# Kernel optimization log

Hardware: AMD Instinct MI355X
Metric: run time of the kernel (lower is better)

Reference implementation:

```python
import jax, jax.numpy as jnp
import numpy as np

N = 50000          # nodes
E = 1250000        # edges (no self loops in raw data)
H = 2              # heads
C = 32             # out channels per head
DIN = 64           # dim_node
ED = 16            # edge_dim
G = 16             # graphs in batch
NC = 5             # num classes
SLOPE = 0.2        # GATConv leaky_relu negative_slope


def _glorot(key, shape):
    fan = shape[0] if len(shape) == 2 else shape[-1]
    return jax.random.normal(key, shape, jnp.float32) * (1.0 / np.sqrt(fan))


def setup_inputs() -> dict:
    key = jax.random.key(0)
    ks = jax.random.split(key, 24)
    x = jax.random.normal(ks[0], (N, DIN), jnp.float32)
    dst = jax.random.randint(ks[1], (E,), 0, N)
    off = jax.random.randint(ks[2], (E,), 1, N)
    src = (dst + off) % N  # guarantees src != dst (PyG removes self loops before re-adding)
    edge_index = jnp.stack([src, dst]).astype(jnp.int32)
    edge_attr = jax.random.normal(ks[3], (E, ED), jnp.float32)
    batch = jnp.sort(jax.random.randint(ks[4], (N,), 0, G)).astype(jnp.int32)
    inp = dict(x=x, edge_index=edge_index, edge_attr=edge_attr, batch=batch)
    # layer 1: in=DIN, heads=H, out=C, concat -> H*C
    inp["W1"] = _glorot(ks[5], (DIN, H * C)); inp["asrc1"] = _glorot(ks[6], (H, C))
    inp["adst1"] = _glorot(ks[7], (H, C)); inp["We1"] = _glorot(ks[8], (ED, H * C))
    inp["ae1"] = _glorot(ks[9], (H, C)); inp["b1"] = jnp.zeros((H * C,), jnp.float32)
    # layer 2: in=H*C, heads=H, out=C, concat
    inp["W2"] = _glorot(ks[10], (H * C, H * C)); inp["asrc2"] = _glorot(ks[11], (H, C))
    inp["adst2"] = _glorot(ks[12], (H, C)); inp["We2"] = _glorot(ks[13], (ED, H * C))
    inp["ae2"] = _glorot(ks[14], (H, C)); inp["b2"] = jnp.zeros((H * C,), jnp.float32)
    # layer 3: in=H*C, heads=1, out=C, concat=False
    inp["W3"] = _glorot(ks[15], (H * C, C)); inp["asrc3"] = _glorot(ks[16], (1, C))
    inp["adst3"] = _glorot(ks[17], (1, C)); inp["We3"] = _glorot(ks[18], (ED, C))
    inp["ae3"] = _glorot(ks[19], (1, C)); inp["b3"] = jnp.zeros((C,), jnp.float32)
    # ffn: Linear(C, NC) + softmax (dropout is identity in eval)
    inp["Wf"] = _glorot(ks[20], (C, NC)); inp["bf"] = jnp.zeros((NC,), jnp.float32)
    return inp


def _gat_layer(h_in, src, dst, eattr, W, asrc, adst, We, ae, b, heads, out, concat):
    n = h_in.shape[0]
    h = (h_in @ W).reshape(n, heads, out)                      # [N,H,C]
    s_src = jnp.einsum('nhc,hc->nh', h, asrc)                  # per-node src scores
    s_dst = jnp.einsum('nhc,hc->nh', h, adst)
    he = (eattr @ We).reshape(-1, heads, out)                  # [E,H,C]
    s_e = jnp.einsum('ehc,hc->eh', he, ae)
    logit = jax.nn.leaky_relu(s_src[src] + s_dst[dst] + s_e, SLOPE)  # [E,H]
    m = jax.ops.segment_max(logit, dst, num_segments=n)
    ex = jnp.exp(logit - m[dst])
    den = jax.ops.segment_sum(ex, dst, num_segments=n)
    alpha = ex / (den[dst] + 1e-16)                            # segment softmax per dst node
    agg = jax.ops.segment_sum(h[src] * alpha[..., None], dst, num_segments=n)  # [N,H,C]
    out_x = agg.reshape(n, heads * out) if concat else agg.mean(axis=1)
    return out_x + b


def _gat_forward(x, edge_index, edge_attr, batch,
                 W1, asrc1, adst1, We1, ae1, b1,
                 W2, asrc2, adst2, We2, ae2, b2,
                 W3, asrc3, adst3, We3, ae3, b3,
                 Wf, bf):
    src, dst = edge_index[0], edge_index[1]
    n = x.shape[0]
    # add_self_loops with fill_value='mean': self-loop edge_attr = mean of incoming edge_attr
    deg = jax.ops.segment_sum(jnp.ones((src.shape[0],), x.dtype), dst, num_segments=n)
    self_attr = jax.ops.segment_sum(edge_attr, dst, num_segments=n) / jnp.maximum(deg, 1.0)[:, None]
    loop = jnp.arange(n, dtype=src.dtype)
    src_a = jnp.concatenate([src, loop])
    dst_a = jnp.concatenate([dst, loop])
    eattr_a = jnp.concatenate([edge_attr, self_attr], axis=0)

    h = jax.nn.relu(_gat_layer(x, src_a, dst_a, eattr_a, W1, asrc1, adst1, We1, ae1, b1, H, C, True))
    h = jax.nn.relu(_gat_layer(h, src_a, dst_a, eattr_a, W2, asrc2, adst2, We2, ae2, b2, H, C, True))
    h = jax.nn.relu(_gat_layer(h, src_a, dst_a, eattr_a, W3, asrc3, adst3, We3, ae3, b3, 1, C, False))

    # global mean pool per graph
    cnt = jax.ops.segment_sum(jnp.ones((n,), h.dtype), batch, num_segments=G)
    pooled = jax.ops.segment_sum(h, batch, num_segments=G) / jnp.maximum(cnt, 1.0)[:, None]
    # ffn: Dropout (identity at eval) -> Linear -> Softmax(dim=1)
    return jax.nn.softmax(pooled @ Wf + bf, axis=1)


def reference(x, edge_index, edge_attr, batch,
              W1, asrc1, adst1, We1, ae1, b1,
              W2, asrc2, adst2, We2, ae2, b2,
              W3, asrc3, adst3, We3, ae3, b3,
              Wf, bf):
    return _gat_forward(x, edge_index, edge_attr, batch,
                        W1, asrc1, adst1, We1, ae1, b1,
                        W2, asrc2, adst2, We2, ae2, b2,
                        W3, asrc3, adst3, We3, ae3, b3,
                        Wf, bf)
```

## Files before the change

kernel.cpp:

```cpp
#include <hip/hip_runtime.h>
#include <math.h>

#define NN 50000
#define EE 1250000
#define GG 16
#define NCLS 5
#define NBIN 391
#define BINSHIFT 7
#define CAPB 3900

constexpr size_t AL(size_t x){ return (x + 255) & ~size_t(255); }
constexpr size_t OFF_ROWPTR = 0;
constexpr size_t OFF_CURS   = OFF_ROWPTR + AL((size_t)(NN+1)*4);
constexpr size_t OFF_SRCS   = OFF_CURS + AL(4096);
constexpr size_t OFF_SE12   = OFF_SRCS + AL((size_t)EE*2);
constexpr size_t OFF_SE34   = OFF_SE12 + AL((size_t)EE*4);
constexpr size_t OFF_SE5    = OFF_SE34 + AL((size_t)EE*4);
constexpr size_t OFF_SSRC   = OFF_SE5 + AL((size_t)EE*2);
constexpr size_t OFF_SDST   = OFF_SSRC + AL((size_t)NN*2*4);
constexpr size_t OFF_STAG   = OFF_SDST + AL((size_t)NN*2*4);
constexpr size_t OFF_BUFH   = OFF_STAG + AL((size_t)NBIN*CAPB*16);
constexpr size_t OFF_BUFO   = OFF_BUFH + AL((size_t)NN*32*4);
constexpr size_t OFF_WEFF   = OFF_BUFO + AL((size_t)NN*64*4);
constexpr size_t OFF_POOL   = OFF_WEFF + AL(80*4);

__device__ __forceinline__ float leaky(float x){ return x > 0.f ? x : 0.2f*x; }
__device__ __forceinline__ unsigned rne_bf16(float x){
    unsigned u = __float_as_uint(x);
    return (u + 0x7FFFu + ((u >> 16) & 1u)) >> 16;
}
__device__ __forceinline__ float bf16lo(unsigned p){ return __uint_as_float(p << 16); }
__device__ __forceinline__ float bf16hi(unsigned p){ return __uint_as_float(p & 0xFFFF0000u); }

__global__ void weffbinit_kernel(const float* __restrict__ We1, const float* __restrict__ ae1,
                                 const float* __restrict__ We2, const float* __restrict__ ae2,
                                 const float* __restrict__ We3, const float* __restrict__ ae3,
                                 float* __restrict__ weff, int* __restrict__ bincursor){
    int t = threadIdx.x;
    if (t < NBIN) bincursor[t] = t*CAPB;
    if (t >= 80) return;
    int j = t >> 4, d = t & 15;
    const float* We; const float* ae; int hc, h;
    if (j == 0){ We = We1; ae = ae1; hc = 64; h = 0; }
    else if (j == 1){ We = We1; ae = ae1; hc = 64; h = 1; }
    else if (j == 2){ We = We2; ae = ae2; hc = 64; h = 0; }
    else if (j == 3){ We = We2; ae = ae2; hc = 64; h = 1; }
    else { We = We3; ae = ae3; hc = 32; h = 0; }
    float s = 0.f;
    for (int c = 0; c < 32; ++c) s += We[d*hc + h*32 + c] * ae[h*32 + c];
    weff[j*16 + d] = s;
}

__global__ void binA_kernel(const int* __restrict__ src, const int* __restrict__ dst,
                            const float* __restrict__ eattr, const float* __restrict__ weff,
                            int* __restrict__ bincursor, int4* __restrict__ staging, int nE){
    __shared__ int lcount[NBIN];
    __shared__ int lbase[NBIN];
    __shared__ float w[80];
    int tid = threadIdx.x;
    if (tid < 80) w[tid] = weff[tid];
    for (int i = tid; i < NBIN; i += 1024) lcount[i] = 0;
    __syncthreads();
    int base = blockIdx.x * 2048;
    int w0[2], bn[2], idx[2]; unsigned p01[2], p23[2], p4[2];
    #pragma unroll
    for (int k = 0; k < 2; ++k){
        int i = base + k*1024 + tid;
        if (i < nE){
            int d = dst[i];
            int s = src[i];
            bn[k]  = d >> BINSHIFT;
            w0[k]  = s | ((d & 127) << 16);
            const float4* row = (const float4*)(eattr + (size_t)i*16);
            float4 a0 = row[0], a1 = row[1], a2 = row[2], a3 = row[3];
            float a[16] = {a0.x,a0.y,a0.z,a0.w, a1.x,a1.y,a1.z,a1.w,
                           a2.x,a2.y,a2.z,a2.w, a3.x,a3.y,a3.z,a3.w};
            float sj[5];
            #pragma unroll
            for (int j = 0; j < 5; ++j){
                float s2 = 0.f;
                #pragma unroll
                for (int d2 = 0; d2 < 16; ++d2) s2 += a[d2]*w[j*16+d2];
                sj[j] = s2;
            }
            p01[k] = rne_bf16(sj[0]) | (rne_bf16(sj[1]) << 16);
            p23[k] = rne_bf16(sj[2]) | (rne_bf16(sj[3]) << 16);
            p4[k]  = rne_bf16(sj[4]);
            idx[k] = atomicAdd(&lcount[bn[k]], 1);
        } else bn[k] = -1;
    }
    __syncthreads();
    for (int i = tid; i < NBIN; i += 1024)
        lbase[i] = atomicAdd(&bincursor[i], lcount[i]);
    __syncthreads();
    #pragma unroll
    for (int k = 0; k < 2; ++k)
        if (bn[k] >= 0)
            staging[lbase[bn[k]] + idx[k]] = make_int4(w0[k], (int)p01[k], (int)p23[k], (int)p4[k]);
}

__global__ void binscan_kernel(const int* __restrict__ bincursor, int* __restrict__ binbase){
    __shared__ int s[512];
    int tid = threadIdx.x;
    int v = (tid < NBIN) ? (bincursor[tid] - tid*CAPB) : 0;
    s[tid] = v;
    __syncthreads();
    for (int off = 1; off < 512; off <<= 1){
        int t = (tid >= off) ? s[tid-off] : 0;
        __syncthreads();
        s[tid] += t;
        __syncthreads();
    }
    if (tid < NBIN) binbase[tid] = s[tid] - v;
}

__global__ void binB_kernel(const int* __restrict__ bincursor, const int* __restrict__ binbase,
                            const int4* __restrict__ staging,
                            unsigned short* __restrict__ srcs, unsigned* __restrict__ se12,
                            unsigned* __restrict__ se34, unsigned short* __restrict__ se5,
                            int* __restrict__ rowptr, int nN){
    __shared__ int4 lout[CAPB];
    __shared__ int lcnt[128];
    __shared__ int lpre[128];
    int b = blockIdx.x;
    int sbase = b*CAPB;
    int cnt = bincursor[b] - sbase;
    int tid = threadIdx.x;
    if (tid < 128) lcnt[tid] = 0;
    __syncthreads();
    for (int k = tid; k < cnt; k += 1024)
        atomicAdd(&lcnt[staging[sbase + k].x >> 16], 1);
    __syncthreads();
    if (tid < 64){
        int a0 = lcnt[2*tid], a1 = lcnt[2*tid+1];
        int pair = a0 + a1, incl = pair;
        #pragma unroll
        for (int off = 1; off < 64; off <<= 1){
            int t = __shfl_up(incl, off);
            if (tid >= off) incl += t;
        }
        int base0 = incl - pair;
        lpre[2*tid] = base0;
        lpre[2*tid+1] = base0 + a0;
    }
    __syncthreads();
    int r0 = binbase[b];
    int lo = b << BINSHIFT;
    if (tid < 128 && lo + tid < nN) rowptr[lo + tid] = r0 + lpre[tid];
    if (b == NBIN-1 && tid == 0) rowptr[nN] = r0 + cnt;
    if (tid < 128) lcnt[tid] = 0;
    __syncthreads();
    for (int k = tid; k < cnt; k += 1024){
        int4 v = staging[sbase + k];
        int dl = v.x >> 16;
        int rank = atomicAdd(&lcnt[dl], 1);
        v.x &= 0xFFFF;
        lout[lpre[dl] + rank] = v;
    }
    __syncthreads();
    for (int k = tid; k < cnt; k += 1024){
        int4 v = lout[k];
        srcs[r0 + k] = (unsigned short)v.x;
        se12[r0 + k] = (unsigned)v.y;
        se34[r0 + k] = (unsigned)v.z;
        se5[r0 + k]  = (unsigned short)v.w;
    }
}

template<int OUTC>
__global__ void transform_kernel(const float* __restrict__ in, const float* __restrict__ W,
                                 const float* __restrict__ asrc, const float* __restrict__ adst,
                                 unsigned* __restrict__ hout2, float* __restrict__ ssrc,
                                 float* __restrict__ sdst, int nN){
    constexpr int R = 256/OUTC;
    __shared__ float Ws[64*OUTC];
    __shared__ float ins[R*64];
    int tid = threadIdx.x;
    for (int i = tid; i < 64*OUTC; i += 256) Ws[i] = W[i];
    int base = blockIdx.x * R;
    for (int i = tid; i < R*64; i += 256){
        int n = base + i/64;
        ins[i] = (n < nN) ? in[(size_t)n*64 + (i & 63)] : 0.f;
    }
    __syncthreads();
    int r = tid / OUTC, c = tid % OUTC;
    int n = base + r;
    float acc = 0.f;
    #pragma unroll
    for (int d = 0; d < 64; ++d) acc += ins[r*64 + d] * Ws[d*OUTC + c];
    float ps = acc * asrc[c];
    float pd = acc * adst[c];
    #pragma unroll
    for (int m = 1; m <= 16; m <<= 1){ ps += __shfl_xor(ps, m); pd += __shfl_xor(pd, m); }
    float accN = __shfl_xor(acc, 1);
    if (n < nN){
        int h = c >> 5;
        if ((c & 1) == 0){
            unsigned pk = rne_bf16(acc) | (rne_bf16(accN) << 16);
            hout2[((size_t)h*nN + n)*16 + ((c & 31) >> 1)] = pk;
        }
        if ((c & 31) == 0){
            ssrc[(size_t)h*nN + n] = ps;
            sdst[(size_t)h*nN + n] = pd;
        }
    }
}

template<int MODE>
__global__ void aggH_kernel(const int* __restrict__ rowptr, const unsigned short* __restrict__ srcs,
                            const unsigned* __restrict__ sePa, const unsigned short* __restrict__ sePb,
                            const float* __restrict__ ssrcH, const float* __restrict__ sdstH,
                            const uint2* __restrict__ hb2, const float* __restrict__ bias,
                            float4* __restrict__ outb, int ostride4, int nN){
    int wid = threadIdx.x >> 6;
    int lane = threadIdx.x & 63;
    int n = blockIdx.x*4 + wid;
    if (n >= nN) return;
    int row_start = rowptr[n], row_end = rowptr[n+1];
    int degn = row_end - row_start;
    float sdh = sdstH[n];
    int q0 = lane >> 3, lc = lane & 7;

    float acc0=0.f, acc1=0.f, acc2=0.f, acc3=0.f, den=0.f, ssp=0.f;
    for (int p0 = row_start; p0 < row_end; p0 += 64){
        int myp = p0 + lane;
        unsigned wpk = 0;
        if (myp < row_end){
            int srcreg = srcs[myp];
            float e;
            if (MODE == 0)      e = __uint_as_float(((unsigned)sePb[myp]) << 16);
            else if (MODE == 1) e = bf16lo(sePa[myp]);
            else                e = bf16hi(sePa[myp]);
            ssp += e;
            float wv = __expf(leaky(ssrcH[srcreg] + sdh + e));
            wpk = (unsigned)srcreg | (rne_bf16(wv) << 16);
        }
        int cnt2 = min(64, row_end - p0);
        for (int qq = q0; qq < cnt2; qq += 8){
            unsigned u = __shfl(wpk, qq);
            int sj = u & 0xFFFF;
            float wj = __uint_as_float(u & 0xFFFF0000u);
            den += wj;
            uint2 hv = hb2[(size_t)sj*8 + lc];
            acc0 += wj * bf16lo(hv.x);
            acc1 += wj * bf16hi(hv.x);
            acc2 += wj * bf16lo(hv.y);
            acc3 += wj * bf16hi(hv.y);
        }
    }
    #pragma unroll
    for (int m = 1; m < 64; m <<= 1) ssp += __shfl_xor(ssp, m);
    #pragma unroll
    for (int m = 8; m < 64; m <<= 1){
        acc0 += __shfl_xor(acc0, m); acc1 += __shfl_xor(acc1, m);
        acc2 += __shfl_xor(acc2, m); acc3 += __shfl_xor(acc3, m);
        den  += __shfl_xor(den, m);
    }
    float invdeg = 1.f / (float)max(degn, 1);
    float wself = __expf(leaky(ssrcH[n] + sdh + ssp*invdeg));
    uint2 hv = hb2[(size_t)n*8 + lc];
    acc0 += wself * bf16lo(hv.x); acc1 += wself * bf16hi(hv.x);
    acc2 += wself * bf16lo(hv.y); acc3 += wself * bf16hi(hv.y);
    den += wself;
    if (lane < 8){
        float inv = 1.f / (den + 1e-16f);
        float4 o;
        o.x = fmaxf(acc0*inv + bias[4*lc+0], 0.f);
        o.y = fmaxf(acc1*inv + bias[4*lc+1], 0.f);
        o.z = fmaxf(acc2*inv + bias[4*lc+2], 0.f);
        o.w = fmaxf(acc3*inv + bias[4*lc+3], 0.f);
        outb[(size_t)n*ostride4 + lc] = o;
    }
}

__global__ void pool_kernel(const float* __restrict__ h3, const int* __restrict__ batch,
                            float* __restrict__ pool, float* __restrict__ cnt, int nN){
    __shared__ float accs[GG*32];
    __shared__ float acccnt[GG];
    int tid = threadIdx.x;
    for (int i = tid; i < GG*32; i += 256) accs[i] = 0.f;
    if (tid < GG) acccnt[tid] = 0.f;
    __syncthreads();
    int r = tid >> 5, c = tid & 31;
    int base = blockIdx.x * 512;
    int end = min(base + 512, nN);
    for (int n = base + r; n < end; n += 8){
        int g = batch[n];
        atomicAdd(&accs[g*32 + c], h3[(size_t)n*32 + c]);
        if (c == 0) atomicAdd(&acccnt[g], 1.f);
    }
    __syncthreads();
    for (int i = tid; i < GG*32; i += 256) atomicAdd(&pool[i], accs[i]);
    if (tid < GG) atomicAdd(&cnt[tid], acccnt[tid]);
}

__global__ void final_kernel(const float* __restrict__ pool, const float* __restrict__ cnt,
                             const float* __restrict__ Wf, const float* __restrict__ bf,
                             float* __restrict__ out){
    int g = threadIdx.x;
    if (g >= GG) return;
    float ic = 1.f / fmaxf(cnt[g], 1.f);
    float lg[NCLS];
    #pragma unroll
    for (int k = 0; k < NCLS; ++k) lg[k] = bf[k];
    for (int c = 0; c < 32; ++c){
        float v = pool[g*32 + c] * ic;
        #pragma unroll
        for (int k = 0; k < NCLS; ++k) lg[k] += v * Wf[c*NCLS + k];
    }
    float mx = lg[0];
    #pragma unroll
    for (int k = 1; k < NCLS; ++k) mx = fmaxf(mx, lg[k]);
    float sum = 0.f, ex[NCLS];
    #pragma unroll
    for (int k = 0; k < NCLS; ++k){ ex[k] = expf(lg[k] - mx); sum += ex[k]; }
    #pragma unroll
    for (int k = 0; k < NCLS; ++k) out[g*NCLS + k] = ex[k]/sum;
}

extern "C" void kernel_launch(void* const* d_in, const int* in_sizes, int n_in,
                              void* d_out, int out_size, void* d_ws, size_t ws_size,
                              hipStream_t stream){
    const float* x     = (const float*)d_in[0];
    const int*   eidx  = (const int*)d_in[1];
    const float* eattr = (const float*)d_in[2];
    const int*   batch = (const int*)d_in[3];
    const float* W1 = (const float*)d_in[4];  const float* asrc1 = (const float*)d_in[5];
    const float* adst1 = (const float*)d_in[6]; const float* We1 = (const float*)d_in[7];
    const float* ae1 = (const float*)d_in[8];  const float* b1 = (const float*)d_in[9];
    const float* W2 = (const float*)d_in[10]; const float* asrc2 = (const float*)d_in[11];
    const float* adst2 = (const float*)d_in[12]; const float* We2 = (const float*)d_in[13];
    const float* ae2 = (const float*)d_in[14]; const float* b2 = (const float*)d_in[15];
    const float* W3 = (const float*)d_in[16]; const float* asrc3 = (const float*)d_in[17];
    const float* adst3 = (const float*)d_in[18]; const float* We3 = (const float*)d_in[19];
    const float* ae3 = (const float*)d_in[20]; const float* b3 = (const float*)d_in[21];
    const float* Wf = (const float*)d_in[22]; const float* bf = (const float*)d_in[23];
    float* out = (float*)d_out;

    char* ws = (char*)d_ws;
    int*   rowptr = (int*)(ws + OFF_ROWPTR);
    int*   curs   = (int*)(ws + OFF_CURS);
    unsigned short* srcs = (unsigned short*)(ws + OFF_SRCS);
    unsigned* se12 = (unsigned*)(ws + OFF_SE12);
    unsigned* se34 = (unsigned*)(ws + OFF_SE34);
    unsigned short* se5 = (unsigned short*)(ws + OFF_SE5);
    float* ssrc   = (float*)(ws + OFF_SSRC);
    float* sdst   = (float*)(ws + OFF_SDST);
    int4*  staging = (int4*)(ws + OFF_STAG);
    unsigned* bufH = (unsigned*)(ws + OFF_BUFH);
    float* bufO   = (float*)(ws + OFF_BUFO);
    float* weff   = (float*)(ws + OFF_WEFF);
    float* pool   = (float*)(ws + OFF_POOL);
    float* cnt    = pool + GG*32;

    int* bincursor = curs;
    int* binbase   = curs + 512;

    const int* srcA = eidx;
    const int* dstA = eidx + EE;

    hipMemsetAsync(pool, 0, (GG*32 + GG)*4, stream);

    weffbinit_kernel<<<1, 512, 0, stream>>>(We1, ae1, We2, ae2, We3, ae3, weff, bincursor);
    binA_kernel<<<(EE + 2047)/2048, 1024, 0, stream>>>(srcA, dstA, eattr, weff, bincursor, staging, EE);
    binscan_kernel<<<1, 512, 0, stream>>>(bincursor, binbase);
    binB_kernel<<<NBIN, 1024, 0, stream>>>(bincursor, binbase, staging, srcs, se12, se34, se5, rowptr, NN);

    int ngrid4 = (NN + 3)/4;
    int ngrid8 = (NN + 7)/8;
    const uint2* hb = (const uint2*)bufH;
    float4* o4 = (float4*)bufO;
    transform_kernel<64><<<ngrid4, 256, 0, stream>>>(x, W1, asrc1, adst1, bufH, ssrc, sdst, NN);
    aggH_kernel<1><<<ngrid4, 256, 0, stream>>>(rowptr, srcs, se12, nullptr, ssrc,      sdst,      hb,          b1,      o4,     16, NN);
    aggH_kernel<2><<<ngrid4, 256, 0, stream>>>(rowptr, srcs, se12, nullptr, ssrc + NN, sdst + NN, hb + NN*8,   b1 + 32, o4 + 8, 16, NN);
    transform_kernel<64><<<ngrid4, 256, 0, stream>>>(bufO, W2, asrc2, adst2, bufH, ssrc, sdst, NN);
    aggH_kernel<1><<<ngrid4, 256, 0, stream>>>(rowptr, srcs, se34, nullptr, ssrc,      sdst,      hb,          b2,      o4,     16, NN);
    aggH_kernel<2><<<ngrid4, 256, 0, stream>>>(rowptr, srcs, se34, nullptr, ssrc + NN, sdst + NN, hb + NN*8,   b2 + 32, o4 + 8, 16, NN);
    transform_kernel<32><<<ngrid8, 256, 0, stream>>>(bufO, W3, asrc3, adst3, bufH, ssrc, sdst, NN);
    aggH_kernel<0><<<ngrid4, 256, 0, stream>>>(rowptr, srcs, nullptr, se5, ssrc, sdst, hb, b3, o4, 8, NN);
    pool_kernel<<<(NN + 511)/512, 256, 0, stream>>>(bufO, batch, pool, cnt, NN);
    final_kernel<<<1, 64, 0, stream>>>(pool, cnt, Wf, bf, out);
}
```

Measured before the change: 299.2 us.

## Fuse two-head aggregation into one kernel with node-major interleaved layout

Node features and attention scores are now stored node-major with both heads interleaved, so one aggregation kernel handles both heads per node. This replaces two per-head launches per layer, sharing the CSR walk, source-index and edge-score loads, and the exp computation across heads. Each edge is processed by fewer lanes in parallel because the lanes now cover a wider feature row. The edge binning kernel also handles four edges per thread and skips global atomics for empty bins.

```diff
diff --git a/kernel.cpp b/kernel.cpp
--- a/kernel.cpp
+++ b/kernel.cpp
@@ -61,10 +61,10 @@
     if (tid < 80) w[tid] = weff[tid];
     for (int i = tid; i < NBIN; i += 1024) lcount[i] = 0;
     __syncthreads();
-    int base = blockIdx.x * 2048;
-    int w0[2], bn[2], idx[2]; unsigned p01[2], p23[2], p4[2];
-    #pragma unroll
-    for (int k = 0; k < 2; ++k){
+    int base = blockIdx.x * 4096;
+    int w0[4], bn[4], idx[4]; unsigned p01[4], p23[4], p4[4];
+    #pragma unroll
+    for (int k = 0; k < 4; ++k){
         int i = base + k*1024 + tid;
         if (i < nE){
             int d = dst[i];
@@ -90,11 +90,13 @@
         } else bn[k] = -1;
     }
     __syncthreads();
-    for (int i = tid; i < NBIN; i += 1024)
-        lbase[i] = atomicAdd(&bincursor[i], lcount[i]);
-    __syncthreads();
-    #pragma unroll
-    for (int k = 0; k < 2; ++k)
+    for (int i = tid; i < NBIN; i += 1024){
+        int c = lcount[i];
+        lbase[i] = c ? atomicAdd(&bincursor[i], c) : 0;
+    }
+    __syncthreads();
+    #pragma unroll
+    for (int k = 0; k < 4; ++k)
         if (bn[k] >= 0)
             staging[lbase[bn[k]] + idx[k]] = make_int4(w0[k], (int)p01[k], (int)p23[k], (int)p4[k]);
 }
@@ -194,82 +196,115 @@
     for (int m = 1; m <= 16; m <<= 1){ ps += __shfl_xor(ps, m); pd += __shfl_xor(pd, m); }
     float accN = __shfl_xor(acc, 1);
     if (n < nN){
-        int h = c >> 5;
         if ((c & 1) == 0){
             unsigned pk = rne_bf16(acc) | (rne_bf16(accN) << 16);
-            hout2[((size_t)h*nN + n)*16 + ((c & 31) >> 1)] = pk;
+            hout2[(size_t)n*(OUTC/2) + (c >> 1)] = pk;
         }
+        constexpr int HEADS = OUTC/32;
         if ((c & 31) == 0){
-            ssrc[(size_t)h*nN + n] = ps;
-            sdst[(size_t)h*nN + n] = pd;
+            int h = c >> 5;
+            ssrc[n*HEADS + h] = ps;
+            sdst[n*HEADS + h] = pd;
         }
     }
 }
 
-template<int MODE>
-__global__ void aggH_kernel(const int* __restrict__ rowptr, const unsigned short* __restrict__ srcs,
-                            const unsigned* __restrict__ sePa, const unsigned short* __restrict__ sePb,
-                            const float* __restrict__ ssrcH, const float* __restrict__ sdstH,
-                            const uint2* __restrict__ hb2, const float* __restrict__ bias,
-                            float4* __restrict__ outb, int ostride4, int nN){
+template<int OUTC>
+__global__ void agg_kernel(const int* __restrict__ rowptr, const unsigned short* __restrict__ srcs,
+                           const unsigned* __restrict__ sePa, const unsigned short* __restrict__ sePb,
+                           const float* __restrict__ ssrc, const float* __restrict__ sdst,
+                           const unsigned* __restrict__ hbuf2, const float* __restrict__ bias,
+                           float* __restrict__ outbuf, int nN){
+    constexpr int HEADS = OUTC/32;
+    constexpr int HALF  = OUTC/4;
+    constexpr int EPI   = 64/HALF;
     int wid = threadIdx.x >> 6;
     int lane = threadIdx.x & 63;
     int n = blockIdx.x*4 + wid;
     if (n >= nN) return;
     int row_start = rowptr[n], row_end = rowptr[n+1];
     int degn = row_end - row_start;
-    float sdh = sdstH[n];
-    int q0 = lane >> 3, lc = lane & 7;
-
-    float acc0=0.f, acc1=0.f, acc2=0.f, acc3=0.f, den=0.f, ssp=0.f;
+    float sd0 = sdst[n*HEADS + 0];
+    float sd1 = (HEADS == 2) ? sdst[n*HEADS + 1] : 0.f;
+
+    int sub = lane / HALF;
+    int lc  = lane & (HALF - 1);
+    int h   = (HEADS == 2) ? ((4*lc) >> 5) : 0;
+
+    float acc0=0.f, acc1=0.f, acc2=0.f, acc3=0.f, den=0.f;
+    float ssp0=0.f, ssp1=0.f;
+    const uint2* hb2 = (const uint2*)hbuf2;
+
     for (int p0 = row_start; p0 < row_end; p0 += 64){
         int myp = p0 + lane;
-        unsigned wpk = 0;
+        int srcreg = 0; unsigned wpk = 0; float w0s = 0.f;
         if (myp < row_end){
-            int srcreg = srcs[myp];
-            float e;
-            if (MODE == 0)      e = __uint_as_float(((unsigned)sePb[myp]) << 16);
-            else if (MODE == 1) e = bf16lo(sePa[myp]);
-            else                e = bf16hi(sePa[myp]);
-            ssp += e;
-            float wv = __expf(leaky(ssrcH[srcreg] + sdh + e));
-            wpk = (unsigned)srcreg | (rne_bf16(wv) << 16);
+            srcreg = srcs[myp];
+            if (HEADS == 2){
+                unsigned pk = sePa[myp];
+                float e0 = bf16lo(pk);
+                float e1 = bf16hi(pk);
+                ssp0 += e0; ssp1 += e1;
+                float2 sv = ((const float2*)ssrc)[srcreg];
+                float w0 = __expf(leaky(sv.x + sd0 + e0));
+                float w1 = __expf(leaky(sv.y + sd1 + e1));
+                wpk = rne_bf16(w0) | (rne_bf16(w1) << 16);
+            } else {
+                float e0 = __uint_as_float(((unsigned)sePb[myp]) << 16);
+                ssp0 += e0;
+                w0s = __expf(leaky(ssrc[srcreg] + sd0 + e0));
+            }
         }
-        int cnt2 = min(64, row_end - p0);
-        for (int qq = q0; qq < cnt2; qq += 8){
-            unsigned u = __shfl(wpk, qq);
-            int sj = u & 0xFFFF;
-            float wj = __uint_as_float(u & 0xFFFF0000u);
+        int cnt = min(64, row_end - p0);
+        #pragma unroll 2
+        for (int q = sub; q < cnt; q += EPI){
+            int sj = __shfl(srcreg, q);
+            float wj;
+            if (HEADS == 2){
+                unsigned wq = __shfl(wpk, q);
+                wj = h ? bf16hi(wq) : bf16lo(wq);
+            } else {
+                wj = __shfl(w0s, q);
+            }
             den += wj;
-            uint2 hv = hb2[(size_t)sj*8 + lc];
+            uint2 hv = hb2[(size_t)sj*(OUTC/4) + lc];
             acc0 += wj * bf16lo(hv.x);
             acc1 += wj * bf16hi(hv.x);
             acc2 += wj * bf16lo(hv.y);
             acc3 += wj * bf16hi(hv.y);
         }
     }
-    #pragma unroll
-    for (int m = 1; m < 64; m <<= 1) ssp += __shfl_xor(ssp, m);
-    #pragma unroll
-    for (int m = 8; m < 64; m <<= 1){
+
+    #pragma unroll
+    for (int m = HALF; m < 64; m <<= 1){
         acc0 += __shfl_xor(acc0, m); acc1 += __shfl_xor(acc1, m);
         acc2 += __shfl_xor(acc2, m); acc3 += __shfl_xor(acc3, m);
         den  += __shfl_xor(den, m);
     }
+    #pragma unroll
+    for (int m = 1; m < 64; m <<= 1){
+        ssp0 += __shfl_xor(ssp0, m);
+        if (HEADS == 2) ssp1 += __shfl_xor(ssp1, m);
+    }
+
     float invdeg = 1.f / (float)max(degn, 1);
-    float wself = __expf(leaky(ssrcH[n] + sdh + ssp*invdeg));
-    uint2 hv = hb2[(size_t)n*8 + lc];
+    float srh = ssrc[n*HEADS + h];
+    float sdh = h ? sd1 : sd0;
+    float ssh = h ? ssp1 : ssp0;
+    float wself = __expf(leaky(srh + sdh + ssh*invdeg));
+    uint2 hv = hb2[(size_t)n*(OUTC/4) + lc];
     acc0 += wself * bf16lo(hv.x); acc1 += wself * bf16hi(hv.x);
     acc2 += wself * bf16lo(hv.y); acc3 += wself * bf16hi(hv.y);
     den += wself;
-    if (lane < 8){
+
+    if (lane < HALF){
         float inv = 1.f / (den + 1e-16f);
         float4 o;
         o.x = fmaxf(acc0*inv + bias[4*lc+0], 0.f);
         o.y = fmaxf(acc1*inv + bias[4*lc+1], 0.f);
         o.z = fmaxf(acc2*inv + bias[4*lc+2], 0.f);
         o.w = fmaxf(acc3*inv + bias[4*lc+3], 0.f);
-        outb[(size_t)n*ostride4 + lc] = o;
+        ((float4*)outbuf)[(size_t)n*(OUTC/4) + lc] = o;
     }
 }
 
@@ -362,22 +397,21 @@
     hipMemsetAsync(pool, 0, (GG*32 + GG)*4, stream);
 
     weffbinit_kernel<<<1, 512, 0, stream>>>(We1, ae1, We2, ae2, We3, ae3, weff, bincursor);
-    binA_kernel<<<(EE + 2047)/2048, 1024, 0, stream>>>(srcA, dstA, eattr, weff, bincursor, staging, EE);
+    binA_kernel<<<(EE + 4095)/4096, 1024, 0, stream>>>(srcA, dstA, eattr, weff, bincursor, staging, EE);
     binscan_kernel<<<1, 512, 0, stream>>>(bincursor, binbase);
     binB_kernel<<<NBIN, 1024, 0, stream>>>(bincursor, binbase, staging, srcs, se12, se34, se5, rowptr, NN);
 
     int ngrid4 = (NN + 3)/4;
     int ngrid8 = (NN + 7)/8;
-    const uint2* hb = (const uint2*)bufH;
-    float4* o4 = (float4*)bufO;
     transform_kernel<64><<<ngrid4, 256, 0, stream>>>(x, W1, asrc1, adst1, bufH, ssrc, sdst, NN);
-    aggH_kernel<1><<<ngrid4, 256, 0, stream>>>(rowptr, srcs, se12, nullptr, ssrc,      sdst,      hb,          b1,      o4,     16, NN);
-    aggH_kernel<2><<<ngrid4, 256, 0, stream>>>(rowptr, srcs, se12, nullptr, ssrc + NN, sdst + NN, hb + NN*8,   b1 + 32, o4 + 8, 16, NN);
+    agg_kernel<64><<<ngrid4, 256, 0, stream>>>(rowptr, srcs, se12, nullptr,
+                                               ssrc, sdst, bufH, b1, bufO, NN);
     transform_kernel<64><<<ngrid4, 256, 0, stream>>>(bufO, W2, asrc2, adst2, bufH, ssrc, sdst, NN);
-    aggH_kernel<1><<<ngrid4, 256, 0, stream>>>(rowptr, srcs, se34, nullptr, ssrc,      sdst,      hb,          b2,      o4,     16, NN);
-    aggH_kernel<2><<<ngrid4, 256, 0, stream>>>(rowptr, srcs, se34, nullptr, ssrc + NN, sdst + NN, hb + NN*8,   b2 + 32, o4 + 8, 16, NN);
+    agg_kernel<64><<<ngrid4, 256, 0, stream>>>(rowptr, srcs, se34, nullptr,
+                                               ssrc, sdst, bufH, b2, bufO, NN);
     transform_kernel<32><<<ngrid8, 256, 0, stream>>>(bufO, W3, asrc3, adst3, bufH, ssrc, sdst, NN);
-    aggH_kernel<0><<<ngrid4, 256, 0, stream>>>(rowptr, srcs, nullptr, se5, ssrc, sdst, hb, b3, o4, 8, NN);
+    agg_kernel<32><<<ngrid4, 256, 0, stream>>>(rowptr, srcs, nullptr, se5,
+                                               ssrc, sdst, bufH, b3, bufO, NN);
     pool_kernel<<<(NN + 511)/512, 256, 0, stream>>>(bufO, batch, pool, cnt, NN);
     final_kernel<<<1, 64, 0, stream>>>(pool, cnt, Wf, bf, out);
 }
```

After: 273.2 us. 1.1x faster.
